# Performance work log

Measured on AMD Instinct MI355X. Metric: run time of the kernel, lower is better.

The kernel has to match this reference:

```python
import jax, jax.numpy as jnp
import numpy as np

H_MODEL = 1024
N_HEADS = 16
N_KV_HEADS = 4
HEAD_DIM = 64
SLIDING_WINDOW = 512
B, S = 2, 2048
NEG_INF = -1e9


def rotate_half(x):
    half = x.shape[-1] // 2
    return jnp.concatenate([-x[..., half:], x[..., :half]], axis=-1)


def setup_inputs() -> dict:
    key = jax.random.key(0)
    ks = jax.random.split(key, 8)
    hidden_states = jax.random.normal(ks[0], (B, S, H_MODEL), dtype=jnp.float32)
    # RoPE tables (HF style): cos/sin of shape [1, S, head_dim]
    inv_freq = 1.0 / (10000.0 ** (jnp.arange(0, HEAD_DIM, 2, dtype=jnp.float32) / HEAD_DIM))
    pos = jnp.arange(S, dtype=jnp.float32)
    freqs = jnp.einsum('s,d->sd', pos, inv_freq)            # [S, D/2]
    emb = jnp.concatenate([freqs, freqs], axis=-1)          # [S, D]
    cos = jnp.cos(emb)[None]                                # [1, S, D]
    sin = jnp.sin(emb)[None]
    # additive causal + sliding-window mask [1,1,S,S]
    i = jnp.arange(S)[:, None]
    j = jnp.arange(S)[None, :]
    allowed = (j <= i) & (i - j < SLIDING_WINDOW)
    attention_mask = jnp.where(allowed, 0.0, NEG_INF).astype(jnp.float32)[None, None]
    # projection weights (torch Linear stores [out, in]; y = x @ W.T)
    std = 0.02
    Wq = jax.random.normal(ks[1], (N_HEADS * HEAD_DIM, H_MODEL), dtype=jnp.float32) * std
    Wk = jax.random.normal(ks[2], (N_KV_HEADS * HEAD_DIM, H_MODEL), dtype=jnp.float32) * std
    Wv = jax.random.normal(ks[3], (N_KV_HEADS * HEAD_DIM, H_MODEL), dtype=jnp.float32) * std
    Wo = jax.random.normal(ks[4], (H_MODEL, N_HEADS * HEAD_DIM), dtype=jnp.float32) * std
    return {"hidden_states": hidden_states, "cos": cos, "sin": sin,
            "attention_mask": attention_mask, "Wq": Wq, "Wk": Wk, "Wv": Wv, "Wo": Wo}


def reference(hidden_states, cos, sin, attention_mask, Wq, Wk, Wv, Wo):
    b, s, _ = hidden_states.shape
    G = N_HEADS // N_KV_HEADS
    scaling = HEAD_DIM ** -0.5
    # QKV projections -> [B, H, S, D]
    q = jnp.einsum('bsh,oh->bso', hidden_states, Wq).reshape(b, s, N_HEADS, HEAD_DIM).transpose(0, 2, 1, 3)
    k = jnp.einsum('bsh,oh->bso', hidden_states, Wk).reshape(b, s, N_KV_HEADS, HEAD_DIM).transpose(0, 2, 1, 3)
    v = jnp.einsum('bsh,oh->bso', hidden_states, Wv).reshape(b, s, N_KV_HEADS, HEAD_DIM).transpose(0, 2, 1, 3)
    # RoPE (cos/sin broadcast over head dim via unsqueeze(1))
    c = cos[:, None, :, :]
    sn = sin[:, None, :, :]
    q = q * c + rotate_half(q) * sn
    k = k * c + rotate_half(k) * sn
    # GQA eager attention: group query heads over kv heads
    qg = q.reshape(b, N_KV_HEADS, G, s, HEAD_DIM)
    scores = jnp.einsum('bkgqd,bkpd->bkgqp', qg, k) * scaling  # [B,Hkv,G,S,S]
    scores = scores + attention_mask[:, :, None, :, :]
    probs = jax.nn.softmax(scores.astype(jnp.float32), axis=-1).astype(q.dtype)
    out = jnp.einsum('bkgqp,bkpd->bkgqd', probs, v)            # [B,Hkv,G,S,D]
    out = out.reshape(b, N_HEADS, s, HEAD_DIM).transpose(0, 2, 1, 3).reshape(b, s, N_HEADS * HEAD_DIM)
    return jnp.einsum('bso,ho->bsh', out, Wo)
```

## Files before the change

kernel.cpp:

```cpp
#include <hip/hip_runtime.h>
#include <hip/hip_bf16.h>

#define S_LEN 2048
#define NH 16
#define NKV 4
#define HD 64
#define WIN 512
#define BATCH 2

typedef __bf16 bf16_8 __attribute__((ext_vector_type(8)));
typedef float f32x4 __attribute__((ext_vector_type(4)));

__device__ inline bf16_8 cvt8(f32x4 a, f32x4 b) {
    bf16_8 r;
    r[0] = (__bf16)a[0]; r[1] = (__bf16)a[1]; r[2] = (__bf16)a[2]; r[3] = (__bf16)a[3];
    r[4] = (__bf16)b[0]; r[5] = (__bf16)b[1]; r[6] = (__bf16)b[2]; r[7] = (__bf16)b[3];
    return r;
}

typedef __attribute__((address_space(1))) const unsigned int guint;
typedef __attribute__((address_space(3))) unsigned int luint;
__device__ __forceinline__ void gload16(const void* g, void* l) {
    __builtin_amdgcn_global_load_lds((guint*)g, (luint*)l, 16, 0, 0);
}


__global__ __launch_bounds__(256) void cvt_pack(
    const float* __restrict__ hs, const float* __restrict__ Wq,
    const float* __restrict__ Wk, const float* __restrict__ Wv,
    const float* __restrict__ Wo,
    __bf16* __restrict__ hsp, __bf16* __restrict__ Wqp,
    __bf16* __restrict__ Wkp, __bf16* __restrict__ Wvp,
    __bf16* __restrict__ Wop)
{
    int i = blockIdx.x * 256 + threadIdx.x;
    const float* S; __bf16* P;
    if (i < 524288)      { S = hs; P = hsp; }
    else if (i < 655360) { S = Wq; P = Wqp; i -= 524288; }
    else if (i < 688128) { S = Wk; P = Wkp; i -= 655360; }
    else if (i < 720896) { S = Wv; P = Wvp; i -= 688128; }
    else                 { S = Wo; P = Wop; i -= 720896; }
    const int n = i >> 7;
    const int k = (i & 127) << 3;
    const f32x4 a = *(const f32x4*)(S + (size_t)n * 1024 + k);
    const f32x4 b = *(const f32x4*)(S + (size_t)n * 1024 + k + 4);
    const size_t dst = ((size_t)((n >> 4) * 32 + (k >> 5)) << 9)
                     + ((size_t)((n & 15) | (((k >> 3) & 3) << 4)) << 3);
    *(bf16_8*)(P + dst) = cvt8(a, b);
}

__device__ __forceinline__ void gemm64x128(
    const __bf16* __restrict__ Apk,
    const __bf16* __restrict__ Bp,
    int bx, int colb,
    __bf16* __restrict__ smem,
    int tid, f32x4 acc[2][4])
{
    const int wave = tid >> 6;
    const int lane = tid & 63;
    const int wm   = wave & 1;
    const int wn   = wave >> 1;
    const int lofs = lane << 3;
    const f32x4 fzero = {0.f, 0.f, 0.f, 0.f};
#pragma unroll
    for (int i = 0; i < 2; ++i)
#pragma unroll
        for (int nt = 0; nt < 4; ++nt) acc[i][nt] = fzero;

    const __bf16* aSrc  = Apk + ((size_t)(bx * 4 + wave) * 32) * 512 + lofs;
    const __bf16* bSrc0 = Bp + ((size_t)((colb >> 4) + wave * 2) * 32) * 512 + lofs;
    const __bf16* bSrc1 = Bp + ((size_t)((colb >> 4) + wave * 2 + 1) * 32) * 512 + lofs;

#define STAGE(buf, it) do {                                            \
        __bf16* base = smem + (buf) * 12288;                           \
        gload16(aSrc + (size_t)(it) * 1024,       base + wave * 1024); \
        gload16(aSrc + (size_t)(it) * 1024 + 512, base + wave * 1024 + 512); \
        __bf16* bd = base + 4096 + wave * 2048;                        \
        gload16(bSrc0 + (size_t)(it) * 1024,       bd);                \
        gload16(bSrc0 + (size_t)(it) * 1024 + 512, bd + 512);          \
        gload16(bSrc1 + (size_t)(it) * 1024,       bd + 1024);         \
        gload16(bSrc1 + (size_t)(it) * 1024 + 512, bd + 1536);         \
    } while (0)

    STAGE(0, 0);
    STAGE(1, 1);

#pragma unroll
    for (int it = 0; it < 16; ++it) {
        if (it < 14) STAGE((it + 2) % 3, it + 2);

        if (it < 14)       asm volatile("s_waitcnt vmcnt(12)" ::: "memory");
        else if (it == 14) asm volatile("s_waitcnt vmcnt(6)"  ::: "memory");
        else               asm volatile("s_waitcnt vmcnt(0)"  ::: "memory");
        __builtin_amdgcn_sched_barrier(0);
        __builtin_amdgcn_s_barrier();

        const __bf16* Ab = smem + (it % 3) * 12288;
        const __bf16* Bb = Ab + 4096;
#pragma unroll
        for (int ks = 0; ks < 2; ++ks) {
            bf16_8 af[2], bf[4];
#pragma unroll
            for (int i = 0; i < 2; ++i)
                af[i] = *(const bf16_8*)(Ab + ((wm * 2 + i) * 2 + ks) * 512 + lofs);
#pragma unroll
            for (int nt = 0; nt < 4; ++nt)
                bf[nt] = *(const bf16_8*)(Bb + ((wn * 4 + nt) * 2 + ks) * 512 + lofs);
#pragma unroll
            for (int i = 0; i < 2; ++i)
#pragma unroll
                for (int nt = 0; nt < 4; ++nt)
                    acc[i][nt] = __builtin_amdgcn_mfma_f32_16x16x32_bf16(af[i], bf[nt], acc[i][nt], 0, 0, 0);
        }
        __builtin_amdgcn_s_barrier();
    }
#undef STAGE
}

__global__ __launch_bounds__(256) void gemm_qkv(
    const __bf16* __restrict__ Apk,
    const __bf16* __restrict__ Wqp,
    const __bf16* __restrict__ Wkp,
    const __bf16* __restrict__ Wvp,
    __bf16* __restrict__ Qp,
    __bf16* __restrict__ Kf,
    __bf16* __restrict__ Vf,
    const float* __restrict__ cosb,
    const float* __restrict__ sinb)
{
    __shared__ __align__(16) __bf16 smem[36864];

    const int tid  = threadIdx.x;
    const int wave = tid >> 6;
    const int lane = tid & 63;
    const int wm   = wave & 1;
    const int wn   = wave >> 1;
    const int fm   = lane & 15;

    const int bx   = blockIdx.x;
    const int row0 = bx * 64;
    const int by   = blockIdx.y;

    const __bf16* Bp; int colb; int mode;
    if (by < 8)       { Bp = Wqp; colb = by * 128;        mode = 0; }
    else if (by < 10) { Bp = Wkp; colb = (by - 8) * 128;  mode = 1; }
    else              { Bp = Wvp; colb = (by - 10) * 128; mode = 2; }
    const int col0 = colb;

    f32x4 acc[2][4];
    gemm64x128(Apk, Bp, bx, colb, smem, tid, acc);

    const int drow = (lane >> 4) << 2;
    const int cq   = col0 + wn * 64;
    const int bb   = row0 >> 11;
    const int sk0  = row0 & (S_LEN - 1);

    if (mode == 0) {
        const int lp = drow | ((fm >> 3) << 4);
#pragma unroll
        for (int i = 0; i < 2; ++i) {
            const size_t t1 = (size_t)(bx * 4 + wm * 2 + i) * 32 + (cq >> 5);
#pragma unroll
            for (int r = 0; r < 4; ++r) {
                const int row = row0 + wm * 32 + i * 16 + drow + r;
                const int s   = row & (S_LEN - 1);
#pragma unroll
                for (int nt = 0; nt < 2; ++nt) {
                    const int d = nt * 16 + fm;
                    const float c1 = cosb[s * HD + d];
                    const float s1 = sinb[s * HD + d];
                    const float c2 = cosb[s * HD + d + 32];
                    const float s2 = sinb[s * HD + d + 32];
                    const float x1 = acc[i][nt][r];
                    const float x2 = acc[i][nt + 2][r];
                    const size_t o = ((size_t)(lp + r + (nt * 2 << 4)) << 3) + (fm & 7);
                    Qp[(t1 << 9) + o]       = (__bf16)(x1 * c1 - x2 * s1);
                    Qp[((t1 + 1) << 9) + o] = (__bf16)(x2 * c2 + x1 * s2);
                }
            }
        }
    } else if (mode == 1) {
        __bf16* T = smem;
        __syncthreads();
#pragma unroll
        for (int i = 0; i < 2; ++i) {
#pragma unroll
            for (int r = 0; r < 4; ++r) {
                const int kl = wm * 32 + i * 16 + drow + r;
                const int s  = sk0 + kl;
#pragma unroll
                for (int nt = 0; nt < 2; ++nt) {
                    const int d = nt * 16 + fm;
                    const float c1 = cosb[s * HD + d];
                    const float s1 = sinb[s * HD + d];
                    const float c2 = cosb[s * HD + d + 32];
                    const float s2 = sinb[s * HD + d + 32];
                    const float x1 = acc[i][nt][r];
                    const float x2 = acc[i][nt + 2][r];
                    T[kl * 136 + wn * 64 + d]      = (__bf16)(x1 * c1 - x2 * s1);
                    T[kl * 136 + wn * 64 + d + 32] = (__bf16)(x2 * c2 + x1 * s2);
                }
            }
        }
        __syncthreads();
#pragma unroll
        for (int c = 0; c < 4; ++c) {
            const int tile = c * 4 + wave;
            const int hh  = tile >> 3;
            const int kt4 = (tile >> 1) & 3;
            const int dd  = tile & 1;
            const int key = kt4 * 16 + fm;
            const int dl  = dd * 32 + ((lane >> 4) << 3);
            const bf16_8 v = *(const bf16_8*)&T[key * 136 + hh * 64 + dl];
            const int khg = (col0 + hh * 64) >> 6;
            const int ktg = (sk0 >> 4) + kt4;
            *(bf16_8*)&Kf[(size_t)(bb * NKV + khg) * 131072 + (size_t)(ktg * 2 + dd) * 512 + lane * 8] = v;
        }
    } else {
        __bf16* T2 = smem;
        __syncthreads();
#pragma unroll
        for (int i = 0; i < 2; ++i)
#pragma unroll
            for (int r = 0; r < 4; ++r)
#pragma unroll
                for (int nt = 0; nt < 4; ++nt)
                    T2[(wn * 64 + nt * 16 + fm) * 72 + wm * 32 + i * 16 + drow + r] =
                        (__bf16)acc[i][nt][r];
        __syncthreads();
#pragma unroll
        for (int c = 0; c < 4; ++c) {
            const int tile = c * 4 + wave;
            const int hh  = tile >> 3;
            const int dd4 = (tile >> 1) & 3;
            const int ks  = tile & 1;
            const int dl  = dd4 * 16 + fm;
            const int key = ks * 32 + ((lane >> 4) << 3);
            const bf16_8 v = *(const bf16_8*)&T2[(hh * 64 + dl) * 72 + key];
            const int khg = (col0 + hh * 64) >> 6;
            const int kvg = (sk0 >> 5) + ks;
            *(bf16_8*)&Vf[(size_t)(bb * NKV + khg) * 131072 + (size_t)(dd4 * 64 + kvg) * 512 + lane * 8] = v;
        }
    }
}

__global__ __launch_bounds__(256) void gemm_o(
    const __bf16* __restrict__ Apk,
    const __bf16* __restrict__ Bp,
    float* __restrict__ C)
{
    __shared__ __align__(16) __bf16 smem[36864];

    const int tid  = threadIdx.x;
    const int wave = tid >> 6;
    const int lane = tid & 63;
    const int wm   = wave & 1;
    const int wn   = wave >> 1;

    const int bx   = blockIdx.x;
    const int row0 = bx * 64;
    const int colb = blockIdx.y * 128;

    f32x4 acc[2][4];
    gemm64x128(Apk, Bp, bx, colb, smem, tid, acc);

    const int fm = lane & 15;
    const int drow = (lane >> 4) << 2;
#pragma unroll
    for (int i = 0; i < 2; ++i)
#pragma unroll
        for (int r = 0; r < 4; ++r) {
            const int row = row0 + wm * 32 + i * 16 + drow + r;
#pragma unroll
            for (int nt = 0; nt < 4; ++nt)
                C[(size_t)row * 1024 + colb + wn * 64 + nt * 16 + fm] = acc[i][nt][r];
        }
}

__global__ __launch_bounds__(256) void attn_pk(const __bf16* __restrict__ Qp,
                                               const __bf16* __restrict__ Kf,
                                               const __bf16* __restrict__ Vf,
                                               __bf16* __restrict__ Op)
{
    __shared__ __align__(16) __bf16 Ps[4][16][72];

    const int tid  = threadIdx.x;
    const int wave = tid >> 6;
    const int lane = tid & 63;

    const int bid0 = blockIdx.x;
    const int bid  = (bid0 & 7) * 128 + (bid0 >> 3);

    const int qt = bid & (S_LEN / 64 - 1);
    const int h  = (bid >> 5) & (NH - 1);
    const int b  = bid >> 9;
    const int kh = h >> 2;

    const int q0 = qt * 64;
    const int qw = q0 + wave * 16;

    const int fm = lane & 15;

    const size_t qtile = ((size_t)((b * S_LEN + qw) >> 4) * 32 + h * 2) << 9;
    const bf16_8 qf0 = *(const bf16_8*)&Qp[qtile + (lane << 3)];
    const bf16_8 qf1 = *(const bf16_8*)&Qp[qtile + 512 + (lane << 3)];

    const __bf16* Kfb = Kf + (size_t)(b * NKV + kh) * 131072 + lane * 8;
    const __bf16* Vfb = Vf + (size_t)(b * NKV + kh) * 131072 + lane * 8;

    const f32x4 fzero = {0.f, 0.f, 0.f, 0.f};
    f32x4 oacc[4];
    float l[4];
#pragma unroll
    for (int nt = 0; nt < 4; ++nt) oacc[nt] = fzero;
#pragma unroll
    for (int r = 0; r < 4; ++r) l[r] = 0.f;

    const int qbase = qw + ((lane >> 4) << 2);
    const int fj = (lane >> 4) << 3;

    const int lo  = (qw >= WIN) ? ((qw - WIN + 1) & ~63) : 0;
    const int hi  = (qw + 15) & ~63;
    const int nit = ((hi - lo) >> 6) + 1;

    for (int it = 0; it < nit; ++it) {
        const int kb = lo + (it << 6);

        f32x4 sc[4];
        const int ktb = kb >> 4;
#pragma unroll
        for (int t4 = 0; t4 < 4; ++t4) {
            const bf16_8 k0 = *(const bf16_8*)(Kfb + (size_t)((ktb + t4) * 2) * 512);
            const bf16_8 k1 = *(const bf16_8*)(Kfb + (size_t)((ktb + t4) * 2 + 1) * 512);
            f32x4 s = fzero;
            s = __builtin_amdgcn_mfma_f32_16x16x32_bf16(qf0, k0, s, 0, 0, 0);
            s = __builtin_amdgcn_mfma_f32_16x16x32_bf16(qf1, k1, s, 0, 0, 0);
            sc[t4] = s;
        }

#pragma unroll
        for (int t4 = 0; t4 < 4; ++t4) {
            const int ki = kb + t4 * 16 + fm;
#pragma unroll
            for (int r = 0; r < 4; ++r) {
                const int qr = qbase + r;
                const float e = __expf(sc[t4][r] * 0.125f);
                const float p = (ki <= qr && qr - ki < WIN) ? e : 0.f;
                l[r] += p;
                Ps[wave][((lane >> 4) << 2) + r][t4 * 16 + fm] = (__bf16)p;
            }
        }

        const bf16_8 pf0 = *(const bf16_8*)&Ps[wave][fm][fj];
        const bf16_8 pf1 = *(const bf16_8*)&Ps[wave][fm][32 + fj];

        const int kvb = kb >> 5;
#pragma unroll
        for (int nt = 0; nt < 4; ++nt) {
            const bf16_8 v0 = *(const bf16_8*)(Vfb + (size_t)(nt * 64 + kvb) * 512);
            const bf16_8 v1 = *(const bf16_8*)(Vfb + (size_t)(nt * 64 + kvb + 1) * 512);
            oacc[nt] = __builtin_amdgcn_mfma_f32_16x16x32_bf16(pf0, v0, oacc[nt], 0, 0, 0);
            oacc[nt] = __builtin_amdgcn_mfma_f32_16x16x32_bf16(pf1, v1, oacc[nt], 0, 0, 0);
        }
    }

#pragma unroll
    for (int off = 8; off > 0; off >>= 1)
#pragma unroll
        for (int r = 0; r < 4; ++r)
            l[r] += __shfl_xor(l[r], off, 64);

    const int drow = (lane >> 4) << 2;
    float inv[4];
#pragma unroll
    for (int r = 0; r < 4; ++r) inv[r] = 1.0f / l[r];

    const size_t rt = (size_t)((b * S_LEN + qw) >> 4) * 32;
#pragma unroll
    for (int nt = 0; nt < 4; ++nt) {
        const size_t t = rt + h * 2 + (nt >> 1);
        const int lp0  = drow | (((nt * 2 + (fm >> 3)) & 3) << 4);
        const int e    = fm & 7;
#pragma unroll
        for (int r = 0; r < 4; ++r)
            Op[(t << 9) + ((size_t)(lp0 + r) << 3) + e] = (__bf16)(oacc[nt][r] * inv[r]);
    }
}

extern "C" void kernel_launch(void* const* d_in, const int* in_sizes, int n_in,
                              void* d_out, int out_size, void* d_ws, size_t ws_size,
                              hipStream_t stream)
{
    const float* hs   = (const float*)d_in[0];
    const float* cosb = (const float*)d_in[1];
    const float* sinb = (const float*)d_in[2];
    const float* Wq = (const float*)d_in[4];
    const float* Wk = (const float*)d_in[5];
    const float* Wv = (const float*)d_in[6];
    const float* Wo = (const float*)d_in[7];

    const int M = BATCH * S_LEN;

    __bf16* hsp = (__bf16*)d_ws;
    __bf16* Wqp = hsp + (size_t)M * 1024;
    __bf16* Wkp = Wqp + 1024 * 1024;
    __bf16* Wvp = Wkp + 256 * 1024;
    __bf16* Wop = Wvp + 256 * 1024;
    __bf16* Qpb = Wop + 1024 * 1024;
    __bf16* Kfb = Qpb + (size_t)M * 1024;
    __bf16* Vfb = Kfb + (size_t)8 * 131072;
    __bf16* Opb = Vfb + (size_t)8 * 131072;

    dim3 blk(256);
    cvt_pack<<<3328, blk, 0, stream>>>(hs, Wq, Wk, Wv, Wo,
                                       hsp, Wqp, Wkp, Wvp, Wop);

    gemm_qkv<<<dim3(64, 12), blk, 0, stream>>>(hsp, Wqp, Wkp, Wvp,
                                               Qpb, Kfb, Vfb, cosb, sinb);

    attn_pk<<<BATCH * NH * (S_LEN / 64), blk, 0, stream>>>(Qpb, Kfb, Vfb, Opb);

    gemm_o<<<dim3(64, 8), blk, 0, stream>>>(Opb, Wop, (float*)d_out);
}
```

Measured before the change: 154.5 us.

## Process two 16-row query tiles per wave to reuse K/V fragment loads

Each wave of the attention kernel now handles 32 query rows as two 16-row tiles that share every K and V fragment loaded from global memory. This roughly halves K/V load traffic per query row and interleaves independent MFMA chains. The grid shrinks to 512 blocks of 128 queries, and register and LDS use per wave grows. The K range per wave widens slightly, which adds some fully masked work at tile boundaries.

Measured after the change: 160.5 us. 3.9% more time.

```diff
diff --git a/kernel.cpp b/kernel.cpp
--- a/kernel.cpp
+++ b/kernel.cpp
@@ -282,60 +282,65 @@
                                                const __bf16* __restrict__ Vf,
                                                __bf16* __restrict__ Op)
 {
-    __shared__ __align__(16) __bf16 Ps[4][16][72];
+    __shared__ __align__(16) __bf16 Ps[4][2][16][72];
 
     const int tid  = threadIdx.x;
     const int wave = tid >> 6;
     const int lane = tid & 63;
 
     const int bid0 = blockIdx.x;
-    const int bid  = (bid0 & 7) * 128 + (bid0 >> 3);
-
-    const int qt = bid & (S_LEN / 64 - 1);
-    const int h  = (bid >> 5) & (NH - 1);
-    const int b  = bid >> 9;
+    const int bid  = (bid0 & 7) * 64 + (bid0 >> 3);
+
+    const int qt = bid & 15;
+    const int h  = (bid >> 4) & (NH - 1);
+    const int b  = bid >> 8;
     const int kh = h >> 2;
 
-    const int q0 = qt * 64;
-    const int qw = q0 + wave * 16;
+    const int q0 = qt * 128;
+    const int qw = q0 + wave * 32;
 
     const int fm = lane & 15;
-
-    const size_t qtile = ((size_t)((b * S_LEN + qw) >> 4) * 32 + h * 2) << 9;
-    const bf16_8 qf0 = *(const bf16_8*)&Qp[qtile + (lane << 3)];
-    const bf16_8 qf1 = *(const bf16_8*)&Qp[qtile + 512 + (lane << 3)];
+    const int fj = (lane >> 4) << 3;
+
+    const size_t qtA = ((size_t)((b * S_LEN + qw) >> 4) * 32 + h * 2) << 9;
+    const bf16_8 qfA0 = *(const bf16_8*)&Qp[qtA + (lane << 3)];
+    const bf16_8 qfA1 = *(const bf16_8*)&Qp[qtA + 512 + (lane << 3)];
+    const bf16_8 qfB0 = *(const bf16_8*)&Qp[qtA + 16384 + (lane << 3)];
+    const bf16_8 qfB1 = *(const bf16_8*)&Qp[qtA + 16384 + 512 + (lane << 3)];
 
     const __bf16* Kfb = Kf + (size_t)(b * NKV + kh) * 131072 + lane * 8;
     const __bf16* Vfb = Vf + (size_t)(b * NKV + kh) * 131072 + lane * 8;
 
     const f32x4 fzero = {0.f, 0.f, 0.f, 0.f};
-    f32x4 oacc[4];
-    float l[4];
-#pragma unroll
-    for (int nt = 0; nt < 4; ++nt) oacc[nt] = fzero;
-#pragma unroll
-    for (int r = 0; r < 4; ++r) l[r] = 0.f;
-
-    const int qbase = qw + ((lane >> 4) << 2);
-    const int fj = (lane >> 4) << 3;
+    f32x4 oaccA[4], oaccB[4];
+    float lA[4], lB[4];
+#pragma unroll
+    for (int nt = 0; nt < 4; ++nt) { oaccA[nt] = fzero; oaccB[nt] = fzero; }
+#pragma unroll
+    for (int r = 0; r < 4; ++r) { lA[r] = 0.f; lB[r] = 0.f; }
+
+    const int qbA = qw + ((lane >> 4) << 2);
+    const int qbB = qbA + 16;
 
     const int lo  = (qw >= WIN) ? ((qw - WIN + 1) & ~63) : 0;
-    const int hi  = (qw + 15) & ~63;
+    const int hi  = (qw + 31) & ~63;
     const int nit = ((hi - lo) >> 6) + 1;
 
     for (int it = 0; it < nit; ++it) {
         const int kb = lo + (it << 6);
 
-        f32x4 sc[4];
+        f32x4 scA[4], scB[4];
         const int ktb = kb >> 4;
 #pragma unroll
         for (int t4 = 0; t4 < 4; ++t4) {
             const bf16_8 k0 = *(const bf16_8*)(Kfb + (size_t)((ktb + t4) * 2) * 512);
             const bf16_8 k1 = *(const bf16_8*)(Kfb + (size_t)((ktb + t4) * 2 + 1) * 512);
-            f32x4 s = fzero;
-            s = __builtin_amdgcn_mfma_f32_16x16x32_bf16(qf0, k0, s, 0, 0, 0);
-            s = __builtin_amdgcn_mfma_f32_16x16x32_bf16(qf1, k1, s, 0, 0, 0);
-            sc[t4] = s;
+            f32x4 sA = fzero, sB = fzero;
+            sA = __builtin_amdgcn_mfma_f32_16x16x32_bf16(qfA0, k0, sA, 0, 0, 0);
+            sB = __builtin_amdgcn_mfma_f32_16x16x32_bf16(qfB0, k0, sB, 0, 0, 0);
+            sA = __builtin_amdgcn_mfma_f32_16x16x32_bf16(qfA1, k1, sA, 0, 0, 0);
+            sB = __builtin_amdgcn_mfma_f32_16x16x32_bf16(qfB1, k1, sB, 0, 0, 0);
+            scA[t4] = sA; scB[t4] = sB;
         }
 
 #pragma unroll
@@ -343,48 +348,64 @@
             const int ki = kb + t4 * 16 + fm;
 #pragma unroll
             for (int r = 0; r < 4; ++r) {
-                const int qr = qbase + r;
-                const float e = __expf(sc[t4][r] * 0.125f);
-                const float p = (ki <= qr && qr - ki < WIN) ? e : 0.f;
-                l[r] += p;
-                Ps[wave][((lane >> 4) << 2) + r][t4 * 16 + fm] = (__bf16)p;
+                const int row = ((lane >> 4) << 2) + r;
+                const int qrA = qbA + r;
+                const float eA = __expf(scA[t4][r] * 0.125f);
+                const float pA = (ki <= qrA && qrA - ki < WIN) ? eA : 0.f;
+                lA[r] += pA;
+                Ps[wave][0][row][t4 * 16 + fm] = (__bf16)pA;
+                const int qrB = qbB + r;
+                const float eB = __expf(scB[t4][r] * 0.125f);
+                const float pB = (ki <= qrB && qrB - ki < WIN) ? eB : 0.f;
+                lB[r] += pB;
+                Ps[wave][1][row][t4 * 16 + fm] = (__bf16)pB;
             }
         }
 
-        const bf16_8 pf0 = *(const bf16_8*)&Ps[wave][fm][fj];
-        const bf16_8 pf1 = *(const bf16_8*)&Ps[wave][fm][32 + fj];
+        const bf16_8 pfA0 = *(const bf16_8*)&Ps[wave][0][fm][fj];
+        const bf16_8 pfA1 = *(const bf16_8*)&Ps[wave][0][fm][32 + fj];
+        const bf16_8 pfB0 = *(const bf16_8*)&Ps[wave][1][fm][fj];
+        const bf16_8 pfB1 = *(const bf16_8*)&Ps[wave][1][fm][32 + fj];
 
         const int kvb = kb >> 5;
 #pragma unroll
         for (int nt = 0; nt < 4; ++nt) {
             const bf16_8 v0 = *(const bf16_8*)(Vfb + (size_t)(nt * 64 + kvb) * 512);
             const bf16_8 v1 = *(const bf16_8*)(Vfb + (size_t)(nt * 64 + kvb + 1) * 512);
-            oacc[nt] = __builtin_amdgcn_mfma_f32_16x16x32_bf16(pf0, v0, oacc[nt], 0, 0, 0);
-            oacc[nt] = __builtin_amdgcn_mfma_f32_16x16x32_bf16(pf1, v1, oacc[nt], 0, 0, 0);
+            oaccA[nt] = __builtin_amdgcn_mfma_f32_16x16x32_bf16(pfA0, v0, oaccA[nt], 0, 0, 0);
+            oaccB[nt] = __builtin_amdgcn_mfma_f32_16x16x32_bf16(pfB0, v0, oaccB[nt], 0, 0, 0);
+            oaccA[nt] = __builtin_amdgcn_mfma_f32_16x16x32_bf16(pfA1, v1, oaccA[nt], 0, 0, 0);
+            oaccB[nt] = __builtin_amdgcn_mfma_f32_16x16x32_bf16(pfB1, v1, oaccB[nt], 0, 0, 0);
         }
     }
 
 #pragma unroll
     for (int off = 8; off > 0; off >>= 1)
 #pragma unroll
-        for (int r = 0; r < 4; ++r)
-            l[r] += __shfl_xor(l[r], off, 64);
+        for (int r = 0; r < 4; ++r) {
+            lA[r] += __shfl_xor(lA[r], off, 64);
+            lB[r] += __shfl_xor(lB[r], off, 64);
+        }
 
     const int drow = (lane >> 4) << 2;
-    float inv[4];
-#pragma unroll
-    for (int r = 0; r < 4; ++r) inv[r] = 1.0f / l[r];
-
-    const size_t rt = (size_t)((b * S_LEN + qw) >> 4) * 32;
-#pragma unroll
-    for (int nt = 0; nt < 4; ++nt) {
-        const size_t t = rt + h * 2 + (nt >> 1);
-        const int lp0  = drow | (((nt * 2 + (fm >> 3)) & 3) << 4);
-        const int e    = fm & 7;
-#pragma unroll
-        for (int r = 0; r < 4; ++r)
-            Op[(t << 9) + ((size_t)(lp0 + r) << 3) + e] = (__bf16)(oacc[nt][r] * inv[r]);
-    }
+    float invA[4], invB[4];
+#pragma unroll
+    for (int r = 0; r < 4; ++r) { invA[r] = 1.0f / lA[r]; invB[r] = 1.0f / lB[r]; }
+
+#define EPI(oacc, inv, qws) do {                                               \
+        const size_t rt = (size_t)((b * S_LEN + (qws)) >> 4) * 32;             \
+        _Pragma("unroll") for (int nt = 0; nt < 4; ++nt) {                     \
+            const size_t t = rt + h * 2 + (nt >> 1);                           \
+            const int lp0  = drow | (((nt * 2 + (fm >> 3)) & 3) << 4);         \
+            const int e    = fm & 7;                                           \
+            _Pragma("unroll") for (int r = 0; r < 4; ++r)                      \
+                Op[(t << 9) + ((size_t)(lp0 + r) << 3) + e] =                  \
+                    (__bf16)((oacc)[nt][r] * (inv)[r]);                        \
+        } } while (0)
+
+    EPI(oaccA, invA, qw);
+    EPI(oaccB, invB, qw + 16);
+#undef EPI
 }
 
 extern "C" void kernel_launch(void* const* d_in, const int* in_sizes, int n_in,
@@ -418,7 +439,7 @@
     gemm_qkv<<<dim3(64, 12), blk, 0, stream>>>(hsp, Wqp, Wkp, Wvp,
                                                Qpb, Kfb, Vfb, cosb, sinb);
 
-    attn_pk<<<BATCH * NH * (S_LEN / 64), blk, 0, stream>>>(Qpb, Kfb, Vfb, Opb);
+    attn_pk<<<BATCH * NH * (S_LEN / 128), blk, 0, stream>>>(Qpb, Kfb, Vfb, Opb);
 
     gemm_o<<<dim3(64, 8), blk, 0, stream>>>(Opb, Wop, (float*)d_out);
 }
```
